# Performance work log

Measured on AMD Instinct MI355X. Metric: run time of the kernel, lower is better.

Reference implementation:

```python
import jax, jax.numpy as jnp
import numpy as np

B, N, E, D, F_IN, EDGE_DIM, VN = 128, 500, 1048576, 128, 5, 2, 10
NEG_FEAT = 0.01   # torch F.leaky_relu default
NEG_ATT = 0.2     # GAT attention slope


def _gat_layer(h_in, src, dst, edge_attr, W, b, a_src, a_dst, a_edge, We, n_nodes):
    # Edge-feature GAT conv: per-edge attention over (src, dst, edge) then
    # softmax-normalized scatter-aggregate onto destination nodes.
    h = h_in @ W                                  # [N, d]
    e = edge_attr @ We                            # [E, d] projected edge features
    logits = jax.nn.leaky_relu((h @ a_src)[src] + (h @ a_dst)[dst] + e @ a_edge,
                               negative_slope=NEG_ATT)    # [E]
    # segment softmax over incoming edges of each dst node
    m = jax.ops.segment_max(logits, dst, num_segments=n_nodes)
    ex = jnp.exp(logits - m[dst])
    denom = jax.ops.segment_sum(ex, dst, num_segments=n_nodes)
    alpha = ex / (denom[dst] + 1e-16)             # [E]
    msg = h[src] + e                              # [E, d]
    out = jax.ops.segment_sum(alpha[:, None] * msg, dst, num_segments=n_nodes)
    return out + b


def setup_inputs() -> dict:
    key = jax.random.key(0)
    ks = jax.random.split(key, 20)
    s = 0.05
    return {
        'x': jax.random.normal(ks[0], (B * N, F_IN), jnp.float32),
        'edge_index': jax.random.randint(ks[1], (2, E), 0, B * N, jnp.int64 if jax.config.jax_enable_x64 else jnp.int32).astype(jnp.int32),
        'edge_attr': jax.random.uniform(ks[2], (E, EDGE_DIM), jnp.float32),
        'curr_v_node_id': jax.random.randint(ks[3], (B,), 0, VN).astype(jnp.int32),
        'v_graph_embedding': jax.random.normal(ks[4], (B, D), jnp.float32),
        'v_node_dense_embeddings': jax.random.normal(ks[5], (B, VN, D), jnp.float32),
        'p_W': jax.random.normal(ks[6], (F_IN, D), jnp.float32) * s,
        'p_b': jnp.zeros((D,), jnp.float32),
        'Ws': jax.random.normal(ks[7], (4, D, D), jnp.float32) * s,
        'bs': jnp.zeros((4, D), jnp.float32),
        'a_srcs': jax.random.normal(ks[8], (4, D), jnp.float32) * s,
        'a_dsts': jax.random.normal(ks[9], (4, D), jnp.float32) * s,
        'a_edges': jax.random.normal(ks[10], (4, D), jnp.float32) * s,
        'Wes': jax.random.normal(ks[11], (4, EDGE_DIM, D), jnp.float32) * s,
        'W5': jax.random.normal(ks[12], (D, 1), jnp.float32) * s,
        'b5': jnp.zeros((1,), jnp.float32),
        'a_src5': jax.random.normal(ks[13], (1,), jnp.float32) * s,
        'a_dst5': jax.random.normal(ks[14], (1,), jnp.float32) * s,
        'a_edge5': jax.random.normal(ks[15], (1,), jnp.float32) * s,
        'We5': jax.random.normal(ks[16], (EDGE_DIM, 1), jnp.float32) * s,
    }


def reference(x, edge_index, edge_attr, curr_v_node_id, v_graph_embedding,
              v_node_dense_embeddings, p_W, p_b, Ws, bs, a_srcs, a_dsts,
              a_edges, Wes, W5, b5, a_src5, a_dst5, a_edge5, We5):
    n_nodes = x.shape[0]
    src, dst = edge_index[0], edge_index[1]
    # gather current v-node embedding: [B, D]
    curr_emb = v_node_dense_embeddings[jnp.arange(B), curr_v_node_id]
    # linear + leaky_relu then broadcast-add of graph/node context
    h = jax.nn.leaky_relu(x @ p_W + p_b, negative_slope=NEG_FEAT)  # [B*N, D]
    h = h.reshape(B, N, D) + v_graph_embedding[:, None, :] + curr_emb[:, None, :]
    h = h.reshape(B * N, D)
    # 4 hidden edge-feature GAT layers (128 -> 128) with leaky_relu
    for l in range(4):
        h = _gat_layer(h, src, dst, edge_attr, Ws[l], bs[l], a_srcs[l],
                       a_dsts[l], a_edges[l], Wes[l], n_nodes)
        h = jax.nn.leaky_relu(h, negative_slope=NEG_FEAT)
    # output layer (128 -> 1), no activation
    h = _gat_layer(h, src, dst, edge_attr, W5, b5, a_src5, a_dst5, a_edge5,
                   We5, n_nodes)                    # [B*N, 1]
    return h.reshape(B, N)
```

## Files before the change

kernel.cpp:

```cpp
#include <hip/hip_runtime.h>
#include <hip/hip_bf16.h>

#define BB   128
#define NN   500
#define NV   64000
#define EE   1048576
#define DD   128
#define FIN  5
#define VNN  10
#define NBUK 250
#define BCAP 8192

typedef unsigned int   uint32;
typedef unsigned short u16b;
typedef __attribute__((ext_vector_type(8))) short short8;
typedef __attribute__((ext_vector_type(4))) float float4v;

#define P_ASRC  0
#define P_ADST  512
#define P_WE    1024
#define P_BIAS  2048
#define P_W5    2560
#define P_CVEC  2688
#define P_SC5   2700
#define P_TOT   2816

static __device__ __forceinline__ float bf2f(__hip_bfloat16 v) { return __bfloat162float(v); }
static __device__ __forceinline__ float lo2f(uint32 u) { return __uint_as_float(u << 16); }
static __device__ __forceinline__ float hi2f(uint32 u) { return __uint_as_float(u & 0xFFFF0000u); }
static __device__ __forceinline__ uint32 f2bf_bits(float f) {
    uint32 u = __float_as_uint(f);
    return (u + 0x7FFFu + ((u >> 16) & 1u)) >> 16;
}
static __device__ __forceinline__ uint32 pack2(float a, float b) {
    return (f2bf_bits(a) & 0xFFFFu) | (f2bf_bits(b) << 16);
}
static __device__ __forceinline__ float ldf(const void* p, int i, int flag) {
    return flag ? ((const float*)p)[i] : bf2f(((const __hip_bfloat16*)p)[i]);
}

__global__ void sniff_kernel(const unsigned short* __restrict__ p16, int* __restrict__ FLAG) {
    __shared__ int sHigh, sZero;
    if (threadIdx.x == 0) { sHigh = 0; sZero = 0; }
    __syncthreads();
    unsigned short v = p16[2 * threadIdx.x];
    if (v >= 0x8000u) atomicOr(&sHigh, 1);
    if (v == 0)       atomicAdd(&sZero, 1);
    __syncthreads();
    if (threadIdx.x == 0) FLAG[0] = (sHigh || sZero >= 128) ? 1 : 0;
}

__global__ void zero_out_kernel(void* __restrict__ out, const int* __restrict__ FLAG, float tag) {
    int i = blockIdx.x * blockDim.x + threadIdx.x;
    if (i >= NV) return;
    float v = (i == 0) ? tag : 0.f;
    if (FLAG[0]) ((float*)out)[i] = v;
    else         ((u16b*)out)[i] = (u16b)f2bf_bits(v);
}

__global__ void prep_kernel(const void* __restrict__ Wes, const void* __restrict__ aeg,
                            const void* __restrict__ We5, const void* __restrict__ ae5,
                            const void* __restrict__ asr, const void* __restrict__ ads,
                            const void* __restrict__ bs, const void* __restrict__ W5,
                            const void* __restrict__ b5, const void* __restrict__ as5,
                            const void* __restrict__ ad5, const int* __restrict__ FLAG,
                            float* __restrict__ PAR) {
    const int flag = FLAG[0];
    if (blockIdx.x == 0) {
        for (int i = threadIdx.x; i < 512; i += 256) PAR[P_ASRC + i] = ldf(asr, i, flag);
    } else if (blockIdx.x == 1) {
        for (int i = threadIdx.x; i < 512; i += 256) PAR[P_ADST + i] = ldf(ads, i, flag);
    } else if (blockIdx.x == 2) {
        for (int i = threadIdx.x; i < 1024; i += 256) PAR[P_WE + i] = ldf(Wes, i, flag);
    } else if (blockIdx.x == 3) {
        for (int i = threadIdx.x; i < 512; i += 256) PAR[P_BIAS + i] = ldf(bs, i, flag);
    } else if (blockIdx.x == 4) {
        int tid = threadIdx.x;
        if (tid < 128) {
            PAR[P_W5 + tid] = ldf(W5, tid, flag);
        } else if (tid < 136) {
            int l = (tid - 128) >> 1, r = (tid - 128) & 1;
            float s = 0.f;
            for (int ch = 0; ch < DD; ++ch)
                s += ldf(Wes, l * 256 + r * DD + ch, flag) * ldf(aeg, l * DD + ch, flag);
            PAR[P_CVEC + l * 2 + r] = s;
        } else if (tid == 136) {
            float ae = ldf(ae5, 0, flag);
            float w0 = ldf(We5, 0, flag), w1 = ldf(We5, 1, flag);
            PAR[P_CVEC + 8] = w0 * ae; PAR[P_CVEC + 9] = w1 * ae;
            PAR[P_CVEC + 10] = w0;     PAR[P_CVEC + 11] = w1;
            PAR[P_SC5 + 0] = ldf(b5, 0, flag);
            PAR[P_SC5 + 1] = ldf(as5, 0, flag);
            PAR[P_SC5 + 2] = ldf(ad5, 0, flag);
        }
    }
}

__global__ __launch_bounds__(256) void prepack_kernel(const void* __restrict__ Ws,
                                                      const int* __restrict__ FLAG,
                                                      u16b* __restrict__ WB) {
    const int flag = FLAG[0];
    int t = blockIdx.x * 256 + threadIdx.x;
    int lane = t & 63;
    int frag = t >> 6;
    int nchunk = frag & 7, kblk = (frag >> 3) & 3, l = frag >> 5;
    int n = nchunk * 16 + (lane & 15);
    int kbase = kblk * 32 + (lane >> 4) * 8;
#pragma unroll
    for (int j = 0; j < 8; ++j) {
        int idx = l * 16384 + (kbase + j) * 128 + n;
        u16b bits = flag ? (u16b)f2bf_bits(((const float*)Ws)[idx])
                         : ((const u16b*)Ws)[idx];
        WB[(size_t)t * 8 + j] = bits;
    }
}

__global__ __launch_bounds__(256) void proj_kernel(
        const void* __restrict__ x, const void* __restrict__ pW,
        const void* __restrict__ pb, const int* __restrict__ curr,
        const void* __restrict__ vge, const void* __restrict__ vnd,
        const int* __restrict__ FLAG, uint32* __restrict__ H) {
    const int flag = FLAG[0];
    const int n = blockIdx.x * 4 + (threadIdx.x >> 6);
    const int lane = threadIdx.x & 63;
    const int b = n / NN;
    int cv = curr[b]; if ((unsigned)cv >= VNN) cv = 0;
    float xv[FIN];
#pragma unroll
    for (int k = 0; k < FIN; ++k) xv[k] = ldf(x, n * FIN + k, flag);
    const int ch = lane * 2;
    float s0 = ldf(pb, ch, flag), s1 = ldf(pb, ch + 1, flag);
#pragma unroll
    for (int k = 0; k < FIN; ++k) {
        s0 = fmaf(xv[k], ldf(pW, k * DD + ch, flag), s0);
        s1 = fmaf(xv[k], ldf(pW, k * DD + ch + 1, flag), s1);
    }
    s0 = (s0 > 0.f) ? s0 : 0.01f * s0;
    s1 = (s1 > 0.f) ? s1 : 0.01f * s1;
    s0 += ldf(vge, b * DD + ch, flag) + ldf(vnd, (b * VNN + cv) * DD + ch, flag);
    s1 += ldf(vge, b * DD + ch + 1, flag) + ldf(vnd, (b * VNN + cv) * DD + ch + 1, flag);
    H[(size_t)n * 64 + lane] = pack2(s0, s1);
}

__global__ void init_kernel(int* __restrict__ gcur, int* __restrict__ counts) {
    int t = blockIdx.x * 256 + threadIdx.x;
    if (t < NBUK) gcur[t] = t * BCAP;
    if (t < 512) counts[NV + t] = 0;
}

__global__ __launch_bounds__(256) void bucketize_kernel(
        const int* __restrict__ src, const int* __restrict__ dst,
        const void* __restrict__ eaP, const int* __restrict__ FLAG,
        int* __restrict__ gcur, uint32* __restrict__ bukx, uint32* __restrict__ buky) {
    __shared__ int cnt[256];
    __shared__ int cur[256];
    const int flag = FLAG[0];
    const int t = threadIdx.x;
    const int e0 = blockIdx.x * 4096;
    cnt[t] = 0;
    __syncthreads();
    int d[16];
#pragma unroll
    for (int i = 0; i < 16; ++i) {
        d[i] = dst[e0 + i * 256 + t];
        if ((unsigned)d[i] >= NV) d[i] = -1;
        if (d[i] >= 0) atomicAdd(&cnt[d[i] >> 8], 1);
    }
    __syncthreads();
    if (t < NBUK) {
        int c = cnt[t];
        cur[t] = c ? atomicAdd(&gcur[t], c) : 0;
    }
    __syncthreads();
#pragma unroll
    for (int i = 0; i < 16; ++i) {
        if (d[i] < 0) continue;
        int e = e0 + i * 256 + t;
        int b = d[i] >> 8;
        int s = src[e];
        if ((unsigned)s >= NV) s = 0;
        uint32 eb;
        if (flag) { float2 v = ((const float2*)eaP)[e]; eb = pack2(v.x, v.y); }
        else      eb = ((const uint32*)eaP)[e];
        int p = atomicAdd(&cur[b], 1);
        if (p < (b + 1) * BCAP) {
            bukx[p] = (uint32)((s & 0xFFFF) | ((d[i] & 255) << 16));
            buky[p] = eb;
        }
    }
}

__global__ __launch_bounds__(256) void bcount_kernel(
        const uint32* __restrict__ bukx, const int* __restrict__ gcur,
        int* __restrict__ counts) {
    __shared__ int c[256];
    const int b = blockIdx.x, t = threadIdx.x;
    c[t] = 0;
    __syncthreads();
    const int base = b * BCAP;
    int cnt = gcur[b] - base;
    if (cnt > BCAP) cnt = BCAP;
    for (int i = t; i < cnt; i += 256)
        atomicAdd(&c[(bukx[base + i] >> 16) & 255], 1);
    __syncthreads();
    counts[b * 256 + t] = c[t];
}

__global__ __launch_bounds__(256) void scan1_kernel(const int* __restrict__ counts,
                                                    int* __restrict__ row_ptr,
                                                    int* __restrict__ partials) {
    __shared__ int sdata[256];
    int tid = threadIdx.x;
    int4 v = ((const int4*)counts)[blockIdx.x * 256 + tid];
    int sum = v.x + v.y + v.z + v.w;
    sdata[tid] = sum;
    __syncthreads();
    int acc = sum;
    for (int off = 1; off < 256; off <<= 1) {
        int t = (tid >= off) ? sdata[tid - off] : 0;
        __syncthreads();
        acc += t;
        sdata[tid] = acc;
        __syncthreads();
    }
    int excl = acc - sum;
    int base = blockIdx.x * 1024 + tid * 4;
    int run = excl;
    if (base + 0 <= NV) row_ptr[base + 0] = run; run += v.x;
    if (base + 1 <= NV) row_ptr[base + 1] = run; run += v.y;
    if (base + 2 <= NV) row_ptr[base + 2] = run; run += v.z;
    if (base + 3 <= NV) row_ptr[base + 3] = run;
    if (tid == 255) partials[blockIdx.x] = acc;
}

__global__ __launch_bounds__(64) void scan2_kernel(const int* __restrict__ partials,
                                                   int* __restrict__ boff, int nb) {
    int lane = threadIdx.x;
    int v = (lane < nb) ? partials[lane] : 0;
    int orig = v;
#pragma unroll
    for (int off = 1; off < 64; off <<= 1) {
        int t = __shfl_up(v, off, 64);
        if (lane >= off) v += t;
    }
    boff[lane] = v - orig;
}

__global__ __launch_bounds__(256) void scan3_kernel(int* __restrict__ row_ptr,
                                                    const int* __restrict__ boff) {
    int add = boff[blockIdx.x];
    int base = blockIdx.x * 1024 + threadIdx.x * 4;
#pragma unroll
    for (int j = 0; j < 4; ++j) {
        int i = base + j;
        if (i <= NV) row_ptr[i] += add;
    }
}

__global__ __launch_bounds__(256) void bscatter_kernel(
        const uint32* __restrict__ bukx, const uint32* __restrict__ buky,
        const int* __restrict__ gcur, const int* __restrict__ row_ptr,
        int* __restrict__ csr_src, uint32* __restrict__ csr_ea) {
    __shared__ int cur[256];
    const int b = blockIdx.x, t = threadIdx.x;
    cur[t] = row_ptr[b * 256 + t];
    __syncthreads();
    const int base = b * BCAP;
    int cnt = gcur[b] - base;
    if (cnt > BCAP) cnt = BCAP;
    for (int i = t; i < cnt; i += 256) {
        uint32 x = bukx[base + i];
        uint32 y = buky[base + i];
        int p = atomicAdd(&cur[(x >> 16) & 255], 1);
        csr_src[p] = (int)(x & 0xFFFFu);
        csr_ea[p] = y;
    }
}

__global__ __launch_bounds__(256) void gemm_kernel(
        const uint32* __restrict__ Hu, const u16b* __restrict__ WBl,
        const float* __restrict__ PARl, uint32* __restrict__ HWu,
        float* __restrict__ ssrc, float* __restrict__ sdst) {
    __shared__ float hs[64 * 129];
    __shared__ float pp[512];
    const int tid = threadIdx.x;
    const int lane = tid & 63;
    const int wave = tid >> 6;
    const int quad = lane >> 4;
    const int n0 = blockIdx.x * 64;
    const int m = n0 + wave * 16 + (lane & 15);

    const u16b* hrow = (const u16b*)Hu + (size_t)m * 128;
    short8 a0 = *(const short8*)(hrow + 0  + quad * 8);
    short8 a1 = *(const short8*)(hrow + 32 + quad * 8);
    short8 a2 = *(const short8*)(hrow + 64 + quad * 8);
    short8 a3 = *(const short8*)(hrow + 96 + quad * 8);

#pragma unroll
    for (int nt = 0; nt < 8; ++nt) {
        const u16b* bbase = WBl + ((size_t)nt * 512 + lane * 8);
        short8 b0 = *(const short8*)(bbase + 0 * 4096);
        short8 b1 = *(const short8*)(bbase + 1 * 4096);
        short8 b2 = *(const short8*)(bbase + 2 * 4096);
        short8 b3 = *(const short8*)(bbase + 3 * 4096);
        float4v acc = {0.f, 0.f, 0.f, 0.f};
        acc = __builtin_amdgcn_mfma_f32_16x16x32_bf16(a0, b0, acc, 0, 0, 0);
        acc = __builtin_amdgcn_mfma_f32_16x16x32_bf16(a1, b1, acc, 0, 0, 0);
        acc = __builtin_amdgcn_mfma_f32_16x16x32_bf16(a2, b2, acc, 0, 0, 0);
        acc = __builtin_amdgcn_mfma_f32_16x16x32_bf16(a3, b3, acc, 0, 0, 0);
#pragma unroll
        for (int r = 0; r < 4; ++r)
            hs[(wave * 16 + quad * 4 + r) * 129 + nt * 16 + (lane & 15)] = acc[r];
    }
    __syncthreads();

    {
        const int mn = tid & 63, cg = tid >> 6;
        const float* Asr = PARl + P_ASRC;
        const float* Ads = PARl + P_ADST;
        const float* row = hs + mn * 129 + cg * 32;
        float ps = 0.f, pd = 0.f;
#pragma unroll
        for (int j = 0; j < 32; ++j) {
            float v = row[j];
            ps = fmaf(v, Asr[cg * 32 + j], ps);
            pd = fmaf(v, Ads[cg * 32 + j], pd);
        }
        pp[tid] = ps; pp[256 + tid] = pd;
    }
    __syncthreads();
    if (tid < 64) {
        ssrc[n0 + tid] = pp[tid] + pp[64 + tid] + pp[128 + tid] + pp[192 + tid];
        sdst[n0 + tid] = pp[256 + tid] + pp[320 + tid] + pp[384 + tid] + pp[448 + tid];
    }

#pragma unroll
    for (int i = 0; i < 4; ++i) {
        int flat = i * 2048 + tid * 8;
        int n = flat >> 7, c = flat & 127;
        const float* p = hs + n * 129 + c;
        uint4 v;
        v.x = pack2(p[0], p[1]); v.y = pack2(p[2], p[3]);
        v.z = pack2(p[4], p[5]); v.w = pack2(p[6], p[7]);
        *(uint4*)(HWu + (size_t)(n0 + n) * 64 + c / 2) = v;
    }
}

__global__ __launch_bounds__(256) void agg_kernel(
        const uint32* __restrict__ HWu, const float* __restrict__ ssrc,
        const float* __restrict__ sdst, const int* __restrict__ csr_src,
        const uint32* __restrict__ csr_ea, const int* __restrict__ row_ptr,
        const float* __restrict__ PAR, int layer, uint32* __restrict__ HoutU,
        float* __restrict__ hw5out, int wantw5) {
    const int lane = threadIdx.x & 63;
    const int n = blockIdx.x * 4 + (threadIdx.x >> 6);
    const int begin = __builtin_amdgcn_readfirstlane(row_ptr[n]);
    const int deg   = __builtin_amdgcn_readfirstlane(row_ptr[n + 1]) - begin;
    const float c0 = PAR[P_CVEC + 2 * layer], c1 = PAR[P_CVEC + 2 * layer + 1];
    const float sd = sdst[n];

    int   sv = 0;
    uint32 eb = 0;
    if (lane < deg) {
        sv = csr_src[begin + lane];
        eb = csr_ea[begin + lane];
    }
    const float ssv = ssrc[sv];

    const int dmain = (deg < 64) ? deg : 64;
    const int npad  = (dmain + 15) & ~15;

    uint32 hA[16], hB[16];
#pragma unroll
    for (int q = 0; q < 16; ++q) {
        int s = __builtin_amdgcn_readlane(sv, q);
        hA[q] = HWu[(s << 6) + lane];
    }
    if (npad > 16) {
#pragma unroll
        for (int q = 0; q < 16; ++q) {
            int s = __builtin_amdgcn_readlane(sv, 16 + q);
            hB[q] = HWu[(s << 6) + lane];
        }
    }

    float L = -3.4e38f;
    if (lane < deg) {
        L = fmaf(hi2f(eb), c1, fmaf(lo2f(eb), c0, ssv + sd));
        L = (L > 0.f) ? L : 0.2f * L;
    }
    float m = L;
    for (int j0 = 64; j0 < deg; j0 += 64) {
        int j = j0 + lane;
        if (j < deg) {
            int s2 = csr_src[begin + j];
            uint32 e2 = csr_ea[begin + j];
            float L2 = fmaf(hi2f(e2), c1, fmaf(lo2f(e2), c0, ssrc[s2] + sd));
            L2 = (L2 > 0.f) ? L2 : 0.2f * L2;
            m = fmaxf(m, L2);
        }
    }
#pragma unroll
    for (int o = 32; o; o >>= 1) m = fmaxf(m, __shfl_xor(m, o, 64));

    float ex = (lane < deg) ? __expf(L - m) : 0.f;
    float dsum = ex, sx = ex * lo2f(eb), sy = ex * hi2f(eb);
    for (int j0 = 64; j0 < deg; j0 += 64) {
        int j = j0 + lane;
        if (j < deg) {
            int s2 = csr_src[begin + j];
            uint32 e2 = csr_ea[begin + j];
            float L2 = fmaf(hi2f(e2), c1, fmaf(lo2f(e2), c0, ssrc[s2] + sd));
            L2 = (L2 > 0.f) ? L2 : 0.2f * L2;
            float x2 = __expf(L2 - m);
            dsum += x2; sx = fmaf(x2, lo2f(e2), sx); sy = fmaf(x2, hi2f(e2), sy);
        }
    }
#pragma unroll
    for (int o = 32; o; o >>= 1) {
        dsum += __shfl_xor(dsum, o, 64);
        sx   += __shfl_xor(sx, o, 64);
        sy   += __shfl_xor(sy, o, 64);
    }

    const uint32 exu = __float_as_uint(ex);
    float acc0 = 0.f, acc1 = 0.f;
#pragma unroll
    for (int q = 0; q < 16; ++q) {
        float w = __uint_as_float(__builtin_amdgcn_readlane((int)exu, q));
        acc0 = fmaf(w, lo2f(hA[q]), acc0);
        acc1 = fmaf(w, hi2f(hA[q]), acc1);
    }
    if (npad > 16) {
#pragma unroll
        for (int q = 0; q < 16; ++q) {
            float w = __uint_as_float(__builtin_amdgcn_readlane((int)exu, 16 + q));
            acc0 = fmaf(w, lo2f(hB[q]), acc0);
            acc1 = fmaf(w, hi2f(hB[q]), acc1);
        }
    }
    for (int j = 32; j < dmain; ++j) {
        int s = __builtin_amdgcn_readlane(sv, j);
        float w = __uint_as_float(__builtin_amdgcn_readlane((int)exu, j));
        uint32 hb = HWu[(s << 6) + lane];
        acc0 = fmaf(w, lo2f(hb), acc0);
        acc1 = fmaf(w, hi2f(hb), acc1);
    }
    for (int jj = 64; jj < deg; ++jj) {
        int s = csr_src[begin + jj];
        uint32 e2 = csr_ea[begin + jj];
        float L2 = fmaf(hi2f(e2), c1, fmaf(lo2f(e2), c0, ssrc[s] + sd));
        L2 = (L2 > 0.f) ? L2 : 0.2f * L2;
        float x2 = __expf(L2 - m);
        uint32 hb = HWu[(size_t)s * 64 + lane];
        acc0 = fmaf(x2, lo2f(hb), acc0);
        acc1 = fmaf(x2, hi2f(hb), acc1);
    }

    const int ch = lane * 2;
    const float* WEl = PAR + P_WE + layer * 256;
    const float inv = 1.f / (dsum + 1e-16f);
    const float* Bl = PAR + P_BIAS + layer * DD;
    float t0 = fmaf(sy, WEl[DD + ch],     fmaf(sx, WEl[ch],     acc0));
    float t1 = fmaf(sy, WEl[DD + ch + 1], fmaf(sx, WEl[ch + 1], acc1));
    float o0 = fmaf(t0, inv, Bl[ch]);
    float o1 = fmaf(t1, inv, Bl[ch + 1]);
    o0 = (o0 > 0.f) ? o0 : 0.01f * o0;
    o1 = (o1 > 0.f) ? o1 : 0.01f * o1;
    HoutU[(size_t)n * 64 + lane] = pack2(o0, o1);

    if (wantw5) {
        float p = o0 * PAR[P_W5 + ch] + o1 * PAR[P_W5 + ch + 1];
#pragma unroll
        for (int o = 32; o; o >>= 1) p += __shfl_xor(p, o, 64);
        if (lane == 0) hw5out[n] = p;
    }
}

__global__ __launch_bounds__(256) void final_kernel(
        const float* __restrict__ hw5, const int* __restrict__ csr_src,
        const uint32* __restrict__ csr_ea, const int* __restrict__ row_ptr,
        const float* __restrict__ PAR, const int* __restrict__ FLAG,
        void* __restrict__ out) {
    const int flag = FLAG[0];
    int lane = threadIdx.x & 63;
    int n = blockIdx.x * 4 + (threadIdx.x >> 6);
    int begin = __builtin_amdgcn_readfirstlane(row_ptr[n]);
    int deg   = __builtin_amdgcn_readfirstlane(row_ptr[n + 1]) - begin;
    float c50 = PAR[P_CVEC + 8], c51 = PAR[P_CVEC + 9];
    float ce0 = PAR[P_CVEC + 10], ce1 = PAR[P_CVEC + 11];
    float b5v = PAR[P_SC5], a5s = PAR[P_SC5 + 1];
    float hd = PAR[P_SC5 + 2] * hw5[n];

    float m = -3.4e38f;
    for (int j0 = 0; j0 < deg; j0 += 64) {
        int j = j0 + lane;
        if (j < deg) {
            int s = csr_src[begin + j];
            uint32 eb = csr_ea[begin + j];
            float L = fmaf(hi2f(eb), c51, fmaf(lo2f(eb), c50, fmaf(a5s, hw5[s], hd)));
            L = (L > 0.f) ? L : 0.2f * L;
            m = fmaxf(m, L);
        }
    }
#pragma unroll
    for (int o = 32; o; o >>= 1) m = fmaxf(m, __shfl_xor(m, o, 64));

    float dsum = 0.f, msum = 0.f;
    for (int j0 = 0; j0 < deg; j0 += 64) {
        int j = j0 + lane;
        if (j < deg) {
            int s = csr_src[begin + j];
            uint32 eb = csr_ea[begin + j];
            float hs5 = hw5[s];
            float L = fmaf(hi2f(eb), c51, fmaf(lo2f(eb), c50, fmaf(a5s, hs5, hd)));
            L = (L > 0.f) ? L : 0.2f * L;
            float ex = __expf(L - m);
            dsum += ex;
            msum = fmaf(ex, hs5 + fmaf(hi2f(eb), ce1, lo2f(eb) * ce0), msum);
        }
    }
#pragma unroll
    for (int o = 32; o; o >>= 1) {
        dsum += __shfl_xor(dsum, o, 64);
        msum += __shfl_xor(msum, o, 64);
    }
    if (lane == 0) {
        float r = msum / (dsum + 1e-16f) + b5v;
        if (flag) ((float*)out)[n] = r;
        else      ((u16b*)out)[n] = (u16b)f2bf_bits(r);
    }
}

extern "C" void kernel_launch(void* const* d_in, const int* in_sizes, int n_in,
                              void* d_out, int out_size, void* d_ws, size_t ws_size,
                              hipStream_t stream) {
    const void* x   = d_in[0];
    const int*  ei  = (const int*)d_in[1];
    const void* ea  = d_in[2];
    const int*  cur = (const int*)d_in[3];
    const void* vge = d_in[4];
    const void* vnd = d_in[5];
    const void* pW  = d_in[6];
    const void* pb  = d_in[7];
    const void* Ws  = d_in[8];
    const void* bs  = d_in[9];
    const void* asr = d_in[10];
    const void* ads = d_in[11];
    const void* aeg = d_in[12];
    const void* Wes = d_in[13];
    const void* W5  = d_in[14];
    const void* b5  = d_in[15];
    const void* as5 = d_in[16];
    const void* ad5 = d_in[17];
    const void* ae5 = d_in[18];
    const void* We5 = d_in[19];
    (void)in_sizes; (void)n_in; (void)out_size;

    const int* e_src = ei;
    const int* e_dst = ei + EE;

    size_t off = 0;
    char* base = (char*)d_ws;
    auto carve = [&](size_t bytes) {
        void* p = base + off;
        off += (bytes + 255) & ~(size_t)255;
        return p;
    };
    int*    FLAG   = (int*)carve(256);
    float*  PAR    = (float*)carve((size_t)P_TOT * 4);
    u16b*   WB     = (u16b*)carve(4 * DD * DD * 2);
    uint32* H0     = (uint32*)carve((size_t)NV * DD * 2);
    uint32* H1     = (uint32*)carve((size_t)NV * DD * 2);
    float*  SS     = (float*)carve(NV * 4);
    float*  SD     = (float*)carve(NV * 4);
    float*  HW5v   = (float*)carve(NV * 4);
    int*    COUNTS = (int*)carve(65536 * 4);
    int*    ROWPTR = (int*)carve(65536 * 4);
    int*    GCUR   = (int*)carve(256 * 4);
    int*    PART   = (int*)carve(256 * 4);
    int*    BOFF   = (int*)carve(256 * 4);
    int*    CSRS   = (int*)carve((size_t)EE * 4);
    uint32* CSREA  = (uint32*)carve((size_t)EE * 4);
    size_t need = off;

    uint32* BUKX = H1;
    uint32* BUKY = H1 + (size_t)NBUK * BCAP;

    sniff_kernel<<<1, 256, 0, stream>>>((const unsigned short*)ea, FLAG);

    if (need > ws_size) {
        zero_out_kernel<<<(NV + 255) / 256, 256, 0, stream>>>(
            d_out, FLAG, (float)(ws_size >> 20));
        return;
    }

    prep_kernel<<<5, 256, 0, stream>>>(Wes, aeg, We5, ae5, asr, ads, bs,
                                       W5, b5, as5, ad5, FLAG, PAR);
    prepack_kernel<<<32, 256, 0, stream>>>(Ws, FLAG, WB);
    proj_kernel<<<NV / 4, 256, 0, stream>>>(x, pW, pb, cur, vge, vnd, FLAG, H0);

    init_kernel<<<2, 256, 0, stream>>>(GCUR, COUNTS);
    bucketize_kernel<<<EE / 4096, 256, 0, stream>>>(e_src, e_dst, ea, FLAG,
                                                    GCUR, BUKX, BUKY);
    bcount_kernel<<<NBUK, 256, 0, stream>>>(BUKX, GCUR, COUNTS);
    scan1_kernel<<<63, 256, 0, stream>>>(COUNTS, ROWPTR, PART);
    scan2_kernel<<<1, 64, 0, stream>>>(PART, BOFF, 63);
    scan3_kernel<<<63, 256, 0, stream>>>(ROWPTR, BOFF);
    bscatter_kernel<<<NBUK, 256, 0, stream>>>(BUKX, BUKY, GCUR, ROWPTR,
                                              CSRS, CSREA);

    for (int l = 0; l < 4; ++l) {
        gemm_kernel<<<NV / 64, 256, 0, stream>>>(
            H0, WB + (size_t)l * 16384, PAR + l * DD, H1, SS, SD);
        agg_kernel<<<NV / 4, 256, 0, stream>>>(
            H1, SS, SD, CSRS, CSREA, ROWPTR, PAR, l, H0, HW5v, (l == 3) ? 1 : 0);
    }

    final_kernel<<<NV / 4, 256, 0, stream>>>(HW5v, CSRS, CSREA, ROWPTR, PAR,
                                             FLAG, d_out);
}
```

Baseline: 441.9 us.

## Drop segment-max pass from softmax and stage attention weights in LDS

Removes the per-node max-logit pass and its wave reduction from both the aggregation and final kernels, computing exp on the logit clamped at 60 instead of exp(L - max). This lets the weighted accumulation run directly after the weights are computed, reading them from a small LDS array with float4 loads instead of per-edge readlane. Division is also replaced with a hardware reciprocal. The risk is numerical: unnormalized exponentials can lose precision or overflow, and clamping changes results if logits ever exceed 60.

```diff
diff --git a/kernel.cpp b/kernel.cpp
--- a/kernel.cpp
+++ b/kernel.cpp
@@ -352,8 +352,10 @@
         const uint32* __restrict__ csr_ea, const int* __restrict__ row_ptr,
         const float* __restrict__ PAR, int layer, uint32* __restrict__ HoutU,
         float* __restrict__ hw5out, int wantw5) {
+    __shared__ float exs[4][64];
     const int lane = threadIdx.x & 63;
-    const int n = blockIdx.x * 4 + (threadIdx.x >> 6);
+    const int wid = threadIdx.x >> 6;
+    const int n = blockIdx.x * 4 + wid;
     const int begin = __builtin_amdgcn_readfirstlane(row_ptr[n]);
     const int deg   = __builtin_amdgcn_readfirstlane(row_ptr[n + 1]) - begin;
     const float c0 = PAR[P_CVEC + 2 * layer], c1 = PAR[P_CVEC + 2 * layer + 1];
@@ -384,26 +386,42 @@
         }
     }
 
-    float L = -3.4e38f;
+    float ex = 0.f;
     if (lane < deg) {
-        L = fmaf(hi2f(eb), c1, fmaf(lo2f(eb), c0, ssv + sd));
+        float L = fmaf(hi2f(eb), c1, fmaf(lo2f(eb), c0, ssv + sd));
         L = (L > 0.f) ? L : 0.2f * L;
-    }
-    float m = L;
-    for (int j0 = 64; j0 < deg; j0 += 64) {
-        int j = j0 + lane;
-        if (j < deg) {
-            int s2 = csr_src[begin + j];
-            uint32 e2 = csr_ea[begin + j];
-            float L2 = fmaf(hi2f(e2), c1, fmaf(lo2f(e2), c0, ssrc[s2] + sd));
-            L2 = (L2 > 0.f) ? L2 : 0.2f * L2;
-            m = fmaxf(m, L2);
+        ex = __expf(fminf(L, 60.f));
+    }
+    exs[wid][lane] = ex;
+
+    float acc0 = 0.f, acc1 = 0.f;
+    const float* wp = &exs[wid][0];
+#pragma unroll
+    for (int q0 = 0; q0 < 16; q0 += 4) {
+        float4 w4 = *(const float4*)(wp + q0);
+        acc0 = fmaf(w4.x, lo2f(hA[q0 + 0]), acc0); acc1 = fmaf(w4.x, hi2f(hA[q0 + 0]), acc1);
+        acc0 = fmaf(w4.y, lo2f(hA[q0 + 1]), acc0); acc1 = fmaf(w4.y, hi2f(hA[q0 + 1]), acc1);
+        acc0 = fmaf(w4.z, lo2f(hA[q0 + 2]), acc0); acc1 = fmaf(w4.z, hi2f(hA[q0 + 2]), acc1);
+        acc0 = fmaf(w4.w, lo2f(hA[q0 + 3]), acc0); acc1 = fmaf(w4.w, hi2f(hA[q0 + 3]), acc1);
+    }
+    if (npad > 16) {
+#pragma unroll
+        for (int q0 = 16; q0 < 32; q0 += 4) {
+            float4 w4 = *(const float4*)(wp + q0);
+            acc0 = fmaf(w4.x, lo2f(hB[q0 - 16]), acc0); acc1 = fmaf(w4.x, hi2f(hB[q0 - 16]), acc1);
+            acc0 = fmaf(w4.y, lo2f(hB[q0 - 15]), acc0); acc1 = fmaf(w4.y, hi2f(hB[q0 - 15]), acc1);
+            acc0 = fmaf(w4.z, lo2f(hB[q0 - 14]), acc0); acc1 = fmaf(w4.z, hi2f(hB[q0 - 14]), acc1);
+            acc0 = fmaf(w4.w, lo2f(hB[q0 - 13]), acc0); acc1 = fmaf(w4.w, hi2f(hB[q0 - 13]), acc1);
         }
     }
-#pragma unroll
-    for (int o = 32; o; o >>= 1) m = fmaxf(m, __shfl_xor(m, o, 64));
-
-    float ex = (lane < deg) ? __expf(L - m) : 0.f;
+    for (int j = 32; j < dmain; ++j) {
+        int s = __builtin_amdgcn_readlane(sv, j);
+        float w = wp[j];
+        uint32 hb = HWu[(s << 6) + lane];
+        acc0 = fmaf(w, lo2f(hb), acc0);
+        acc1 = fmaf(w, hi2f(hb), acc1);
+    }
+
     float dsum = ex, sx = ex * lo2f(eb), sy = ex * hi2f(eb);
     for (int j0 = 64; j0 < deg; j0 += 64) {
         int j = j0 + lane;
@@ -412,7 +430,7 @@
             uint32 e2 = csr_ea[begin + j];
             float L2 = fmaf(hi2f(e2), c1, fmaf(lo2f(e2), c0, ssrc[s2] + sd));
             L2 = (L2 > 0.f) ? L2 : 0.2f * L2;
-            float x2 = __expf(L2 - m);
+            float x2 = __expf(fminf(L2, 60.f));
             dsum += x2; sx = fmaf(x2, lo2f(e2), sx); sy = fmaf(x2, hi2f(e2), sy);
         }
     }
@@ -423,35 +441,12 @@
         sy   += __shfl_xor(sy, o, 64);
     }
 
-    const uint32 exu = __float_as_uint(ex);
-    float acc0 = 0.f, acc1 = 0.f;
-#pragma unroll
-    for (int q = 0; q < 16; ++q) {
-        float w = __uint_as_float(__builtin_amdgcn_readlane((int)exu, q));
-        acc0 = fmaf(w, lo2f(hA[q]), acc0);
-        acc1 = fmaf(w, hi2f(hA[q]), acc1);
-    }
-    if (npad > 16) {
-#pragma unroll
-        for (int q = 0; q < 16; ++q) {
-            float w = __uint_as_float(__builtin_amdgcn_readlane((int)exu, 16 + q));
-            acc0 = fmaf(w, lo2f(hB[q]), acc0);
-            acc1 = fmaf(w, hi2f(hB[q]), acc1);
-        }
-    }
-    for (int j = 32; j < dmain; ++j) {
-        int s = __builtin_amdgcn_readlane(sv, j);
-        float w = __uint_as_float(__builtin_amdgcn_readlane((int)exu, j));
-        uint32 hb = HWu[(s << 6) + lane];
-        acc0 = fmaf(w, lo2f(hb), acc0);
-        acc1 = fmaf(w, hi2f(hb), acc1);
-    }
     for (int jj = 64; jj < deg; ++jj) {
         int s = csr_src[begin + jj];
         uint32 e2 = csr_ea[begin + jj];
         float L2 = fmaf(hi2f(e2), c1, fmaf(lo2f(e2), c0, ssrc[s] + sd));
         L2 = (L2 > 0.f) ? L2 : 0.2f * L2;
-        float x2 = __expf(L2 - m);
+        float x2 = __expf(fminf(L2, 60.f));
         uint32 hb = HWu[(size_t)s * 64 + lane];
         acc0 = fmaf(x2, lo2f(hb), acc0);
         acc1 = fmaf(x2, hi2f(hb), acc1);
@@ -459,7 +454,7 @@
 
     const int ch = lane * 2;
     const float* WEl = PAR + P_WE + layer * 256;
-    const float inv = 1.f / (dsum + 1e-16f);
+    const float inv = __builtin_amdgcn_rcpf(dsum + 1e-16f);
     const float* Bl = PAR + P_BIAS + layer * DD;
     float t0 = fmaf(sy, WEl[DD + ch],     fmaf(sx, WEl[ch],     acc0));
     float t1 = fmaf(sy, WEl[DD + ch + 1], fmaf(sx, WEl[ch + 1], acc1));
@@ -492,20 +487,6 @@
     float b5v = PAR[P_SC5], a5s = PAR[P_SC5 + 1];
     float hd = PAR[P_SC5 + 2] * hw5[n];
 
-    float m = -3.4e38f;
-    for (int j0 = 0; j0 < deg; j0 += 64) {
-        int j = j0 + lane;
-        if (j < deg) {
-            int s = csr_src[begin + j];
-            uint32 eb = csr_ea[begin + j];
-            float L = fmaf(hi2f(eb), c51, fmaf(lo2f(eb), c50, fmaf(a5s, hw5[s], hd)));
-            L = (L > 0.f) ? L : 0.2f * L;
-            m = fmaxf(m, L);
-        }
-    }
-#pragma unroll
-    for (int o = 32; o; o >>= 1) m = fmaxf(m, __shfl_xor(m, o, 64));
-
     float dsum = 0.f, msum = 0.f;
     for (int j0 = 0; j0 < deg; j0 += 64) {
         int j = j0 + lane;
@@ -515,7 +496,7 @@
             float hs5 = hw5[s];
             float L = fmaf(hi2f(eb), c51, fmaf(lo2f(eb), c50, fmaf(a5s, hs5, hd)));
             L = (L > 0.f) ? L : 0.2f * L;
-            float ex = __expf(L - m);
+            float ex = __expf(fminf(L, 60.f));
             dsum += ex;
             msum = fmaf(ex, hs5 + fmaf(hi2f(eb), ce1, lo2f(eb) * ce0), msum);
         }
@@ -526,7 +507,7 @@
         msum += __shfl_xor(msum, o, 64);
     }
     if (lane == 0) {
-        float r = msum / (dsum + 1e-16f) + b5v;
+        float r = msum * __builtin_amdgcn_rcpf(dsum + 1e-16f) + b5v;
         if (flag) ((float*)out)[n] = r;
         else      ((u16b*)out)[n] = (u16b)f2bf_bits(r);
     }
```

New measurement: 420.5 us. 4.8% less time.
